# Optimization experiments

Hardware: AMD Instinct MI355X
Metric: run time of the kernel (lower is better)

## Reference

```python
import jax, jax.numpy as jnp
import numpy as np

EPS = 1e-6
BN_EPS = 1e-5
K = 20

def vn_linear(x, W):
    # x: (B, Cin, 3, ...), W: (Cout, Cin)
    return jnp.einsum('oc,bc...->bo...', W, x)

def vn_batchnorm(x, gamma, beta):
    # x: (B, C, 3, ...). BN (training-mode batch stats) over per-channel vector norms.
    n = jnp.linalg.norm(x, axis=2) + EPS               # (B, C, ...)
    red = (0,) + tuple(range(2, n.ndim))
    mu = n.mean(red, keepdims=True)
    var = ((n - mu) ** 2).mean(red, keepdims=True)     # biased var, as BatchNorm uses
    sh = (1, -1) + (1,) * (n.ndim - 2)
    nbn = (n - mu) / jnp.sqrt(var + BN_EPS) * gamma.reshape(sh) + beta.reshape(sh)
    return x / n[:, :, None] * nbn[:, :, None]

def vn_leaky(x, Wf, Wd, gamma, beta, ns):
    # VNLinearLeakyReLU: linear -> VN batchnorm -> direction-gated leaky relu
    p = vn_batchnorm(vn_linear(x, Wf), gamma, beta)
    d = vn_linear(x, Wd)
    dot = jnp.sum(p * d, axis=2, keepdims=True)
    dsq = jnp.sum(d * d, axis=2, keepdims=True) + EPS
    neg = p - (dot / dsq) * d
    return ns * p + (1.0 - ns) * jnp.where(dot >= 0, p, neg)

def graph_feature_cross(x, k):
    # x: (B, N, 3) -> edge features (B, 3, 3, N, k): [nbr - x, x, nbr x x]
    sq = jnp.sum(x * x, axis=-1)                        # (B, N)
    d2 = sq[:, :, None] + sq[:, None, :] - 2.0 * jnp.einsum('bnd,bmd->bnm', x, x)
    idx = jax.lax.top_k(-d2, k)[1]                      # (B, N, k) nearest incl. self
    nbr = jax.vmap(lambda pts, ind: pts[ind])(x, idx)   # (B, N, k, 3)
    c = jnp.broadcast_to(x[:, :, None, :], nbr.shape)
    cr = jnp.cross(nbr, c)
    feat = jnp.stack([nbr - c, c, cr], axis=3)          # (B, N, k, 3ch, 3)
    return jnp.transpose(feat, (0, 3, 4, 1, 2))         # (B, 3, 3, N, k)


def setup_inputs() -> dict:
    key = jax.random.key(0)
    ks = iter(jax.random.split(key, 40))
    def W(shape):
        return jax.random.normal(next(ks), shape, jnp.float32) * 0.05
    d = {'x': jax.random.normal(next(ks), (2, 2048, 3), jnp.float32)}
    d.update(
        Wf_pos=W((21, 3)), Wd_pos=W((21, 3)), g_pos=jnp.ones(21), be_pos=jnp.zeros(21),
        Wf1=W((21, 21)), Wd1=W((21, 21)), g1=jnp.ones(21), be1=jnp.zeros(21),
        Wf2=W((42, 21)), Wd2=W((42, 21)), g2=jnp.ones(42), be2=jnp.zeros(42),
        W3=W((170, 42)), g3=jnp.ones(170), be3=jnp.zeros(170),
        Ws1f=W((170, 340)), Ws1d=W((170, 340)), gs1=jnp.ones(170), bs1=jnp.zeros(170),
        Ws2f=W((85, 170)), Ws2d=W((85, 170)), gs2=jnp.ones(85), bs2=jnp.zeros(85),
        Wstd=W((3, 85)),
        Wt1=W((1020, 1020)), Wt2=W((1020, 1020)), Wt3=W((14450, 1020)), bt3=jnp.zeros(14450),
    )
    return d


def reference(x, Wf_pos, Wd_pos, g_pos, be_pos, Wf1, Wd1, g1, be1, Wf2, Wd2, g2, be2,
              W3, g3, be3, Ws1f, Ws1d, gs1, bs1, Ws2f, Ws2d, gs2, bs2, Wstd,
              Wt1, Wt2, Wt3, bt3):
    B, N, _ = x.shape
    feat = graph_feature_cross(x, K)                                   # (B,3,3,N,K)
    h = vn_leaky(feat, Wf_pos, Wd_pos, g_pos, be_pos, 0.0).mean(-1)    # (B,21,3,N) pool over k
    h = vn_leaky(h, Wf1, Wd1, g1, be1, 0.0)                            # (B,21,3,N)
    h = vn_leaky(h, Wf2, Wd2, g2, be2, 0.0)                            # (B,42,3,N)
    h = vn_batchnorm(vn_linear(h, W3), g3, be3)                        # (B,170,3,N)
    z = h.mean(-1)                                                     # (B,170,3)
    h = jnp.concatenate([h, jnp.broadcast_to(z[..., None], z.shape + (N,))], axis=1)  # (B,340,3,N)
    # VNStdFeature (normalize_frame=False, default negative_slope=0.2 inside)
    z0 = vn_leaky(h, Ws1f, Ws1d, gs1, bs1, 0.2)                        # (B,170,3,N)
    z0 = vn_leaky(z0, Ws2f, Ws2d, gs2, bs2, 0.2)                       # (B,85,3,N)
    z0 = vn_linear(z0, Wstd)                                           # (B,3,3,N)
    hs = jnp.einsum('bijn,bjkn->bikn', h, z0)                          # (B,340,3,N) invariant feats
    t = hs.reshape(B, 340 * 3, N)                                      # (B,1020,N)
    t = jax.nn.relu(jnp.einsum('oc,bcn->bon', Wt1, t))
    t = jax.nn.relu(jnp.einsum('oc,bcn->bon', Wt2, t))
    t = jnp.einsum('oc,bcn->bon', Wt3, t) + bt3[None, :, None]         # (B,14450,N)
    theta = t.reshape(B, 85, 170, N)
    return (z, theta)
```

## Files before the change

kernel.cpp:

```cpp
#include <hip/hip_runtime.h>
#include <cstdint>
#include <cstddef>

constexpr int   BB     = 2;
constexpr int   NN     = 2048;
constexpr int   KNB    = 20;
constexpr float EPS_   = 1e-6f;
constexpr float BNEPS_ = 1e-5f;
constexpr int   KPAD   = 1024;
constexpr int   NTK    = KPAD / 64;
constexpr int   MT3    = 57;
constexpr int   MPAD3  = MT3 * 256;

typedef __bf16 bf16x8 __attribute__((ext_vector_type(8)));
typedef float  f32x4  __attribute__((ext_vector_type(4)));

typedef const void t_gvoid __attribute__((address_space(1)));
typedef void       t_lvoid __attribute__((address_space(3)));

__device__ __forceinline__ unsigned short f2bf(float f) {
  unsigned int u = __builtin_bit_cast(unsigned int, f);
  u += 0x7FFFu + ((u >> 16) & 1u);
  return (unsigned short)(u >> 16);
}

__global__ __launch_bounds__(256) void knn_kernel(const float* __restrict__ x,
                                                  int* __restrict__ idx) {
  __shared__ float4 pts[NN];
  const int b = blockIdx.x >> 9;
  const int tid = threadIdx.x;
  const float* xb = x + (size_t)b * NN * 3;
  for (int i = tid; i < NN; i += 256) {
    float px = xb[i * 3], py = xb[i * 3 + 1], pz = xb[i * 3 + 2];
    pts[i] = make_float4(px, py, pz, px * px + py * py + pz * pz);
  }
  __syncthreads();
  const int wave = tid >> 6, lane = tid & 63;
  const int q = (blockIdx.x & 511) * 4 + wave;
  const float4 qp = pts[q];

  float d[32];
  #pragma unroll
  for (int i = 0; i < 32; ++i) {
    const float4 p = pts[lane + 64 * i];
    d[i] = qp.w + p.w - 2.0f * (qp.x * p.x + qp.y * p.y + qp.z * p.z);
  }

  float m; int mi;
  auto rescan = [&]() {
    m = 3.4e38f; mi = 0;
    #pragma unroll
    for (int i = 0; i < 32; ++i)
      if (d[i] < m) { m = d[i]; mi = i; }
  };
  rescan();

  int* op = idx + ((size_t)b * NN + q) * KNB;
  for (int r = 0; r < KNB; ++r) {
    float bm = m; int bj = lane + 64 * mi;
    #pragma unroll
    for (int s = 32; s > 0; s >>= 1) {
      const float om = __shfl_xor(bm, s, 64);
      const int   oj = __shfl_xor(bj, s, 64);
      if (om < bm || (om == bm && oj < bj)) { bm = om; bj = oj; }
    }
    if (lane == 0) op[r] = bj;
    if ((bj & 63) == lane) {
      const int ii = bj >> 6;
      #pragma unroll
      for (int i = 0; i < 32; ++i)
        if (i == ii) d[i] = 3.4e38f;
      rescan();
    }
  }
}

__global__ void feat_kernel(const float* __restrict__ x, const int* __restrict__ idx,
                            float* __restrict__ feat) {
  const int i = blockIdx.x * 256 + threadIdx.x;
  if (i >= BB * NN * KNB) return;
  const int n = (i / KNB) % NN, b = i / (KNB * NN);
  const float* xb = x + (size_t)b * NN * 3;
  const int j = idx[i];
  const float cx = xb[n * 3], cy = xb[n * 3 + 1], cz = xb[n * 3 + 2];
  const float nx = xb[j * 3], ny = xb[j * 3 + 1], nz = xb[j * 3 + 2];
  float* f = feat + (size_t)i * 9;
  f[0] = nx - cx; f[1] = ny - cy; f[2] = nz - cz;
  f[3] = cx;      f[4] = cy;      f[5] = cz;
  f[6] = ny * cz - nz * cy;
  f[7] = nz * cx - nx * cz;
  f[8] = nx * cy - ny * cx;
}

__global__ void l1_stats_part(const float* __restrict__ feat, const float* __restrict__ Wf,
                              float* __restrict__ part) {
  const int o = blockIdx.x, g = blockIdx.y, tid = threadIdx.x;
  const float w0 = Wf[o * 3], w1 = Wf[o * 3 + 1], w2 = Wf[o * 3 + 2];
  const int M = BB * NN * KNB;
  const int chunk = M / 8;
  float s1 = 0.f, s2 = 0.f;
  for (int i = g * chunk + tid; i < (g + 1) * chunk; i += 256) {
    const float* f = feat + (size_t)i * 9;
    float p0 = w0 * f[0] + w1 * f[3] + w2 * f[6];
    float p1 = w0 * f[1] + w1 * f[4] + w2 * f[7];
    float p2 = w0 * f[2] + w1 * f[5] + w2 * f[8];
    float nr = sqrtf(p0 * p0 + p1 * p1 + p2 * p2) + EPS_;
    s1 += nr; s2 += nr * nr;
  }
  __shared__ float rA[256], rB[256];
  rA[tid] = s1; rB[tid] = s2; __syncthreads();
  for (int off = 128; off > 0; off >>= 1) {
    if (tid < off) { rA[tid] += rA[tid + off]; rB[tid] += rB[tid + off]; }
    __syncthreads();
  }
  if (tid == 0) {
    part[(o * 8 + g) * 2]     = rA[0];
    part[(o * 8 + g) * 2 + 1] = rB[0];
  }
}

__global__ void l1_stats_fin(const float* __restrict__ part, const float* __restrict__ gamma,
                             float* __restrict__ stats) {
  const int o = threadIdx.x;
  if (o >= 21) return;
  const int M = BB * NN * KNB;
  float s1 = 0.f, s2 = 0.f;
  for (int g = 0; g < 8; ++g) { s1 += part[(o * 8 + g) * 2]; s2 += part[(o * 8 + g) * 2 + 1]; }
  float mu = s1 / M;
  float var = fmaxf(s2 / M - mu * mu, 0.f);
  stats[2 * o] = mu;
  stats[2 * o + 1] = gamma[o] / sqrtf(var + BNEPS_);
}

__global__ void l1_final_kernel(const float* __restrict__ feat, const float* __restrict__ Wf,
                                const float* __restrict__ Wd, const float* __restrict__ stats,
                                const float* __restrict__ beta, float* __restrict__ h1) {
  const int o = blockIdx.y, b = blockIdx.z;
  const int n = blockIdx.x * 256 + threadIdx.x;
  const float wf0 = Wf[o * 3], wf1 = Wf[o * 3 + 1], wf2 = Wf[o * 3 + 2];
  const float wd0 = Wd[o * 3], wd1 = Wd[o * 3 + 1], wd2 = Wd[o * 3 + 2];
  const float mu = stats[2 * o], sc = stats[2 * o + 1], be = beta[o];
  const float* fb = feat + ((size_t)(b * NN + n)) * KNB * 9;
  float a0 = 0.f, a1 = 0.f, a2 = 0.f;
  for (int k = 0; k < KNB; ++k) {
    const float* f = fb + k * 9;
    float p0 = wf0 * f[0] + wf1 * f[3] + wf2 * f[6];
    float p1 = wf0 * f[1] + wf1 * f[4] + wf2 * f[7];
    float p2 = wf0 * f[2] + wf1 * f[5] + wf2 * f[8];
    float d0 = wd0 * f[0] + wd1 * f[3] + wd2 * f[6];
    float d1 = wd0 * f[1] + wd1 * f[4] + wd2 * f[7];
    float d2 = wd0 * f[2] + wd1 * f[5] + wd2 * f[8];
    float nr = sqrtf(p0 * p0 + p1 * p1 + p2 * p2) + EPS_;
    float fac = ((nr - mu) * sc + be) / nr;
    p0 *= fac; p1 *= fac; p2 *= fac;
    float dot = p0 * d0 + p1 * d1 + p2 * d2;
    if (dot < 0.f) {
      float g = dot / (d0 * d0 + d1 * d1 + d2 * d2 + EPS_);
      p0 -= g * d0; p1 -= g * d1; p2 -= g * d2;
    }
    a0 += p0; a1 += p1; a2 += p2;
  }
  const size_t base = ((size_t)(b * 21 + o) * 3) * NN + n;
  h1[base]          = a0 * (1.f / KNB);
  h1[base + NN]     = a1 * (1.f / KNB);
  h1[base + 2 * NN] = a2 * (1.f / KNB);
}

__global__ void zbias_kernel(const float* __restrict__ zbuf, const float* __restrict__ Wf,
                             const float* __restrict__ Wd, float* __restrict__ zbf,
                             float* __restrict__ zbd, int Cout, int CinFull, int Cz) {
  const int bj = blockIdx.x;
  const int b = bj / 3, j = bj % 3;
  const int o = threadIdx.x;
  if (o >= Cout) return;
  const int off = CinFull - Cz;
  float sf = 0.f, sd = 0.f;
  for (int cz = 0; cz < Cz; ++cz) {
    const float zv = zbuf[((size_t)b * 170 + cz) * 3 + j];
    sf += Wf[(size_t)o * CinFull + off + cz] * zv;
    sd += Wd[(size_t)o * CinFull + off + cz] * zv;
  }
  zbf[(size_t)bj * Cout + o] = sf;
  zbd[(size_t)bj * Cout + o] = sd;
}

template <int HAS_D, int CONCAT_Z>
__global__ __launch_bounds__(256) void vn_lin_fast(
    const float* __restrict__ in, const float* __restrict__ Wf, const float* __restrict__ Wd,
    const float* __restrict__ zbf, const float* __restrict__ zbd,
    float* __restrict__ pout, float* __restrict__ dout,
    int Cin, int CinFull, int Cout) {
  __shared__ float wsh[(HAS_D ? 2 : 1) * 16 * 340];
  float* wfs = wsh;
  float* wds = HAS_D ? (wsh + 16 * 340) : wsh;
  const int tid = threadIdx.x;
  const int nt = blockIdx.x, ot = blockIdx.y;
  const int b = blockIdx.z / 3, j = blockIdx.z % 3;

  for (int i = tid; i < 16 * Cin; i += 256) {
    const int ol = i / Cin, c = i - ol * Cin;
    const int o = ot * 16 + ol;
    wfs[ol * Cin + c] = (o < Cout) ? Wf[(size_t)o * CinFull + c] : 0.f;
    if (HAS_D) wds[ol * Cin + c] = (o < Cout) ? Wd[(size_t)o * CinFull + c] : 0.f;
  }
  __syncthreads();

  const int lane = tid & 63, og = tid >> 6;
  const int n0 = nt * 256 + lane * 4;
  const float* ibase = in + ((size_t)b * Cin * 3 + j) * NN + n0;

  f32x4 accf[4], accd[4];
  #pragma unroll
  for (int oo = 0; oo < 4; ++oo) {
    float bf = 0.f, bd = 0.f;
    if (CONCAT_Z) {
      const int o = ot * 16 + og * 4 + oo;
      if (o < Cout) {
        bf = zbf[(size_t)blockIdx.z * Cout + o];
        bd = zbd[(size_t)blockIdx.z * Cout + o];
      }
    }
    accf[oo] = (f32x4){bf, bf, bf, bf};
    accd[oo] = (f32x4){bd, bd, bd, bd};
  }

  #pragma unroll 4
  for (int c = 0; c < Cin; ++c) {
    const f32x4 v = *reinterpret_cast<const f32x4*>(ibase + (size_t)c * 3 * NN);
    #pragma unroll
    for (int oo = 0; oo < 4; ++oo) {
      const float wf = wfs[(og * 4 + oo) * Cin + c];
      accf[oo] += wf * v;
      if (HAS_D) {
        const float wd = wds[(og * 4 + oo) * Cin + c];
        accd[oo] += wd * v;
      }
    }
  }

  #pragma unroll
  for (int oo = 0; oo < 4; ++oo) {
    const int o = ot * 16 + og * 4 + oo;
    if (o < Cout) {
      const size_t ob = ((size_t)(b * Cout + o) * 3 + j) * NN + n0;
      *reinterpret_cast<f32x4*>(pout + ob) = accf[oo];
      if (HAS_D) *reinterpret_cast<f32x4*>(dout + ob) = accd[oo];
    }
  }
}

__global__ void bn_stats_kernel(const float* __restrict__ p, const float* __restrict__ gamma,
                                float* __restrict__ stats, int Cout) {
  const int o = blockIdx.x, tid = threadIdx.x;
  const int M = BB * NN;
  float s1 = 0.f, s2 = 0.f;
  for (int i = tid; i < M; i += 256) {
    const int b = i >> 11, n = i & (NN - 1);
    const size_t base = (((size_t)(b * Cout + o)) * 3) * NN + n;
    float p0 = p[base], p1 = p[base + NN], p2 = p[base + 2 * NN];
    float nr = sqrtf(p0 * p0 + p1 * p1 + p2 * p2) + EPS_;
    s1 += nr; s2 += nr * nr;
  }
  __shared__ float rA[256], rB[256];
  rA[tid] = s1; rB[tid] = s2; __syncthreads();
  for (int off = 128; off > 0; off >>= 1) {
    if (tid < off) { rA[tid] += rA[tid + off]; rB[tid] += rB[tid + off]; }
    __syncthreads();
  }
  if (tid == 0) {
    float mu = rA[0] / M;
    float var = fmaxf(rB[0] / M - mu * mu, 0.f);
    stats[2 * o] = mu;
    stats[2 * o + 1] = gamma[o] / sqrtf(var + BNEPS_);
  }
}

template <int GATE>
__global__ void vn_gate_kernel(const float* __restrict__ p, const float* __restrict__ d,
                               const float* __restrict__ stats, const float* __restrict__ beta,
                               float* __restrict__ out, int Cout, float ns) {
  const int o = blockIdx.y, b = blockIdx.z;
  const int n = blockIdx.x * 256 + threadIdx.x;
  const size_t base = (((size_t)(b * Cout + o)) * 3) * NN + n;
  float p0 = p[base], p1 = p[base + NN], p2 = p[base + 2 * NN];
  const float nr = sqrtf(p0 * p0 + p1 * p1 + p2 * p2) + EPS_;
  const float fac = ((nr - stats[2 * o]) * stats[2 * o + 1] + beta[o]) / nr;
  p0 *= fac; p1 *= fac; p2 *= fac;
  float o0 = p0, o1 = p1, o2 = p2;
  if (GATE) {
    const float d0 = d[base], d1 = d[base + NN], d2 = d[base + 2 * NN];
    const float dot = p0 * d0 + p1 * d1 + p2 * d2;
    if (dot < 0.f) {
      const float g = dot / (d0 * d0 + d1 * d1 + d2 * d2 + EPS_);
      o0 = p0 - g * d0; o1 = p1 - g * d1; o2 = p2 - g * d2;
    }
    o0 = ns * p0 + (1.f - ns) * o0;
    o1 = ns * p1 + (1.f - ns) * o1;
    o2 = ns * p2 + (1.f - ns) * o2;
  }
  out[base] = o0; out[base + NN] = o1; out[base + 2 * NN] = o2;
}

__global__ void zmean_kernel(const float* __restrict__ h4, float* __restrict__ zbuf,
                             float* __restrict__ outz) {
  const int oj = blockIdx.x;
  const int b = blockIdx.y;
  const int tid = threadIdx.x;
  const float* src = h4 + ((size_t)b * 510 + oj) * NN;
  float s = 0.f;
  for (int n = tid; n < NN; n += 256) s += src[n];
  __shared__ float r[256];
  r[tid] = s; __syncthreads();
  for (int off = 128; off > 0; off >>= 1) {
    if (tid < off) r[tid] += r[tid + off];
    __syncthreads();
  }
  if (tid == 0) {
    float m = r[0] / NN;
    zbuf[(size_t)b * 510 + oj] = m;
    outz[(size_t)b * 510 + oj] = m;
  }
}

__global__ void hs_kernel(const float* __restrict__ h4, const float* __restrict__ zbuf,
                          const float* __restrict__ z0f, unsigned short* __restrict__ t0) {
  const int n = blockIdx.x;
  const int b = blockIdx.z;
  const int tid = threadIdx.x;
  __shared__ float zf[9];
  if (tid < 9) zf[tid] = z0f[(((size_t)(b * 3 + tid / 3)) * 3 + (tid % 3)) * NN + n];
  __syncthreads();
  unsigned short* trow = t0 + ((size_t)b * NN + n) * KPAD;
  for (int c = tid; c < KPAD; c += 256) {
    if (c >= 1020) { trow[c] = 0; continue; }
    const int i = c / 3, kv = c % 3;
    float acc = 0.f;
    #pragma unroll
    for (int j = 0; j < 3; ++j) {
      float hv = (i < 170) ? h4[(((size_t)(b * 170 + i)) * 3 + j) * NN + n]
                           : zbuf[(size_t)b * 510 + (i - 170) * 3 + j];
      acc += hv * zf[j * 3 + kv];
    }
    trow[c] = f2bf(acc);
  }
}

__global__ void wconv_kernel(const float* __restrict__ W, unsigned short* __restrict__ out,
                             int M, int Kv, size_t total) {
  size_t i = (size_t)blockIdx.x * 256 + threadIdx.x;
  const size_t stride = (size_t)gridDim.x * 256;
  for (; i < total; i += stride) {
    const int k = (int)(i & (KPAD - 1));
    const int o = (int)(i >> 10);
    out[i] = (o < M && k < Kv) ? f2bf(W[(size_t)o * Kv + k]) : (unsigned short)0;
  }
}

template <int RELU>
__global__ __launch_bounds__(256) void gemm_kernel(
    const unsigned short* __restrict__ A, const unsigned short* __restrict__ Bmat,
    unsigned short* __restrict__ outB, int M) {
  __shared__ __align__(16) unsigned short lA[2][128 * 64];
  __shared__ __align__(16) unsigned short lB[2][128 * 64];
  const int tid = threadIdx.x;
  const int nwg = gridDim.x, q = nwg >> 3;
  const int orig = blockIdx.x;
  const int swz = (orig & 7) * q + (orig >> 3);
  const int ntile = swz & 15;
  const int mtile = (swz >> 4) & 7;
  const int b = swz >> 7;
  const int lane = tid & 63, w = tid >> 6;
  const int wm = w >> 1, wn = w & 1;
  const int lrow = lane & 15, lgrp = lane >> 4;

  const unsigned short* Abase = A + (size_t)mtile * 128 * KPAD;
  const unsigned short* Bbase = Bmat + ((size_t)b * NN + (size_t)ntile * 128) * KPAD;

  const int rowS = tid >> 3;
  const int scol = ((tid & 7) * 8) ^ ((rowS & 7) * 8);
  const int wb8  = __builtin_amdgcn_readfirstlane(tid & 192) * 8;

  f32x4 acc[4][4];
  #pragma unroll
  for (int mi = 0; mi < 4; ++mi)
    #pragma unroll
    for (int ni = 0; ni < 4; ++ni) acc[mi][ni] = (f32x4){0.f, 0.f, 0.f, 0.f};

  auto stage = [&](int bufi, int kt) {
    const int kof = kt * 64;
    #pragma unroll
    for (int r = 0; r < 4; ++r) {
      __builtin_amdgcn_global_load_lds(
          (t_gvoid*)(Abase + (size_t)(r * 32 + rowS) * KPAD + kof + scol),
          (t_lvoid*)&lA[bufi][r * 2048 + wb8], 16, 0, 0);
      __builtin_amdgcn_global_load_lds(
          (t_gvoid*)(Bbase + (size_t)(r * 32 + rowS) * KPAD + kof + scol),
          (t_lvoid*)&lB[bufi][r * 2048 + wb8], 16, 0, 0);
    }
  };

  stage(0, 0);
  for (int kt = 0; kt < NTK; ++kt) {
    const int cur = kt & 1;
    if (kt + 1 < NTK) {
      stage(cur ^ 1, kt + 1);
      asm volatile("s_waitcnt vmcnt(8)" ::: "memory");
    } else {
      asm volatile("s_waitcnt vmcnt(0)" ::: "memory");
    }
    asm volatile("s_barrier" ::: "memory");

    bf16x8 af[4][2], bfr[4][2];
    #pragma unroll
    for (int mi = 0; mi < 4; ++mi) {
      const int ra = wm * 64 + mi * 16 + lrow;
      const int rb = wn * 64 + mi * 16 + lrow;
      #pragma unroll
      for (int kk = 0; kk < 2; ++kk) {
        af[mi][kk]  = *reinterpret_cast<const bf16x8*>(
            &lA[cur][ra * 64 + ((kk * 32 + lgrp * 8) ^ ((ra & 7) * 8))]);
        bfr[mi][kk] = *reinterpret_cast<const bf16x8*>(
            &lB[cur][rb * 64 + ((kk * 32 + lgrp * 8) ^ ((rb & 7) * 8))]);
      }
    }
    #pragma unroll
    for (int kk = 0; kk < 2; ++kk)
      #pragma unroll
      for (int mi = 0; mi < 4; ++mi)
        #pragma unroll
        for (int ni = 0; ni < 4; ++ni)
          acc[mi][ni] = __builtin_amdgcn_mfma_f32_16x16x32_bf16(af[mi][kk], bfr[ni][kk],
                                                                acc[mi][ni], 0, 0, 0);
    asm volatile("s_barrier" ::: "memory");
  }

  const int fr_col = lane & 15;
  const int fr_rowb = (lane >> 4) * 4;
  #pragma unroll
  for (int mi = 0; mi < 4; ++mi) {
    const int rowb = mtile * 128 + wm * 64 + mi * 16 + fr_rowb;
    #pragma unroll
    for (int ni = 0; ni < 4; ++ni) {
      const int col = ntile * 128 + wn * 64 + ni * 16 + fr_col;
      ushort4 v;
      if (rowb < M) {
        float u0 = acc[mi][ni][0], u1 = acc[mi][ni][1], u2 = acc[mi][ni][2], u3 = acc[mi][ni][3];
        if (RELU) { u0 = fmaxf(u0, 0.f); u1 = fmaxf(u1, 0.f); u2 = fmaxf(u2, 0.f); u3 = fmaxf(u3, 0.f); }
        v.x = f2bf(u0); v.y = f2bf(u1); v.z = f2bf(u2); v.w = f2bf(u3);
      } else {
        v.x = v.y = v.z = v.w = 0;
      }
      *reinterpret_cast<ushort4*>(outB + ((size_t)b * NN + col) * KPAD + rowb) = v;
    }
  }
}

__global__ __launch_bounds__(512, 2) void gemm256_kernel(
    const unsigned short* __restrict__ A, const unsigned short* __restrict__ Bmat,
    float* __restrict__ outF, const float* __restrict__ bias, int M, int MT) {
  __shared__ __align__(16) unsigned short lA[2][256 * 64];
  __shared__ __align__(16) unsigned short lB[2][256 * 64];
  const int tid = threadIdx.x;
  const int nwg = gridDim.x, q = nwg >> 3;
  const int orig = blockIdx.x;
  const int swz = (orig & 7) * q + (orig >> 3);
  const int ntile = swz & 7;
  const int rem = swz >> 3;
  const int mtile = rem % MT;
  const int b = rem / MT;
  const int lane = tid & 63, w = tid >> 6;
  const int wm = w >> 2, wn = w & 3;
  const int lrow = lane & 15, lgrp = lane >> 4;

  const unsigned short* Abase = A + (size_t)mtile * 256 * KPAD;
  const unsigned short* Bbase = Bmat + ((size_t)b * NN + (size_t)ntile * 256) * KPAD;

  const int rowS = tid >> 3;
  const int scol = ((tid & 7) * 8) ^ ((rowS & 7) * 8);
  const int wb8  = __builtin_amdgcn_readfirstlane((tid & 448) >> 6) * 512;

  f32x4 acc[8][4];
  #pragma unroll
  for (int mi = 0; mi < 8; ++mi)
    #pragma unroll
    for (int ni = 0; ni < 4; ++ni) acc[mi][ni] = (f32x4){0.f, 0.f, 0.f, 0.f};

  auto stage = [&](int bufi, int kt) {
    const int kof = kt * 64;
    #pragma unroll
    for (int r = 0; r < 4; ++r) {
      __builtin_amdgcn_global_load_lds(
          (t_gvoid*)(Abase + (size_t)(r * 64 + rowS) * KPAD + kof + scol),
          (t_lvoid*)&lA[bufi][r * 4096 + wb8], 16, 0, 0);
      __builtin_amdgcn_global_load_lds(
          (t_gvoid*)(Bbase + (size_t)(r * 64 + rowS) * KPAD + kof + scol),
          (t_lvoid*)&lB[bufi][r * 4096 + wb8], 16, 0, 0);
    }
  };

  stage(0, 0);
  for (int kt = 0; kt < NTK; ++kt) {
    const int cur = kt & 1;
    if (kt + 1 < NTK) {
      stage(cur ^ 1, kt + 1);
      asm volatile("s_waitcnt vmcnt(8)" ::: "memory");
    } else {
      asm volatile("s_waitcnt vmcnt(0)" ::: "memory");
    }
    asm volatile("s_barrier" ::: "memory");

    #pragma unroll
    for (int kk = 0; kk < 2; ++kk) {
      bf16x8 af[8], bfr[4];
      #pragma unroll
      for (int mi = 0; mi < 8; ++mi) {
        const int ra = wm * 128 + mi * 16 + lrow;
        af[mi] = *reinterpret_cast<const bf16x8*>(
            &lA[cur][ra * 64 + ((kk * 32 + lgrp * 8) ^ ((ra & 7) * 8))]);
      }
      #pragma unroll
      for (int ni = 0; ni < 4; ++ni) {
        const int rb = wn * 64 + ni * 16 + lrow;
        bfr[ni] = *reinterpret_cast<const bf16x8*>(
            &lB[cur][rb * 64 + ((kk * 32 + lgrp * 8) ^ ((rb & 7) * 8))]);
      }
      #pragma unroll
      for (int mi = 0; mi < 8; ++mi)
        #pragma unroll
        for (int ni = 0; ni < 4; ++ni)
          acc[mi][ni] = __builtin_amdgcn_mfma_f32_16x16x32_bf16(af[mi], bfr[ni],
                                                                acc[mi][ni], 0, 0, 0);
    }
    asm volatile("s_barrier" ::: "memory");
  }

  const int fr_col = lane & 15;
  const int fr_rowb = (lane >> 4) * 4;
  #pragma unroll
  for (int mi = 0; mi < 8; ++mi) {
    const int rowb = mtile * 256 + wm * 128 + mi * 16 + fr_rowb;
    #pragma unroll
    for (int ni = 0; ni < 4; ++ni) {
      const int col = ntile * 256 + wn * 64 + ni * 16 + fr_col;
      #pragma unroll
      for (int r = 0; r < 4; ++r) {
        const int rr = rowb + r;
        if (rr < M) outF[((size_t)b * M + rr) * NN + col] = acc[mi][ni][r] + bias[rr];
      }
    }
  }
}

extern "C" void kernel_launch(void* const* d_in, const int* in_sizes, int n_in,
                              void* d_out, int out_size, void* d_ws, size_t ws_size,
                              hipStream_t stream) {
  const float* x      = (const float*)d_in[0];
  const float* Wf_pos = (const float*)d_in[1];
  const float* Wd_pos = (const float*)d_in[2];
  const float* g_pos  = (const float*)d_in[3];
  const float* be_pos = (const float*)d_in[4];
  const float* Wf1    = (const float*)d_in[5];
  const float* Wd1    = (const float*)d_in[6];
  const float* g1     = (const float*)d_in[7];
  const float* be1    = (const float*)d_in[8];
  const float* Wf2    = (const float*)d_in[9];
  const float* Wd2    = (const float*)d_in[10];
  const float* g2     = (const float*)d_in[11];
  const float* be2    = (const float*)d_in[12];
  const float* W3     = (const float*)d_in[13];
  const float* g3     = (const float*)d_in[14];
  const float* be3    = (const float*)d_in[15];
  const float* Ws1f   = (const float*)d_in[16];
  const float* Ws1d   = (const float*)d_in[17];
  const float* gs1    = (const float*)d_in[18];
  const float* bs1    = (const float*)d_in[19];
  const float* Ws2f   = (const float*)d_in[20];
  const float* Ws2d   = (const float*)d_in[21];
  const float* gs2    = (const float*)d_in[22];
  const float* bs2    = (const float*)d_in[23];
  const float* Wstd   = (const float*)d_in[24];
  const float* Wt1    = (const float*)d_in[25];
  const float* Wt2    = (const float*)d_in[26];
  const float* Wt3    = (const float*)d_in[27];
  const float* bt3    = (const float*)d_in[28];
  (void)in_sizes; (void)n_in; (void)out_size; (void)ws_size;

  float* out = (float*)d_out;
  float* out_theta = out + 1020;

  char* ws = (char*)d_ws;
  size_t off = 0;
  auto alloc = [&](size_t bytes) -> void* {
    void* p = (void*)(ws + off);
    off += (bytes + 255) & ~(size_t)255;
    return p;
  };
  int*            idx  = (int*)           alloc((size_t)BB * NN * KNB * 4);
  float*          feat = (float*)         alloc((size_t)BB * NN * KNB * 9 * 4);
  float*          stats= (float*)         alloc(1024 * 4);
  float*          part = (float*)         alloc(2048 * 4);
  float*          h1   = (float*)         alloc((size_t)BB * 21 * 3 * NN * 4);
  float*          h2   = (float*)         alloc((size_t)BB * 21 * 3 * NN * 4);
  float*          h3   = (float*)         alloc((size_t)BB * 42 * 3 * NN * 4);
  float*          h4   = (float*)         alloc((size_t)BB * 170 * 3 * NN * 4);
  float*          zbuf = (float*)         alloc((size_t)BB * 170 * 3 * 4);
  float*          pbuf = (float*)         alloc((size_t)BB * 170 * 3 * NN * 4);
  float*          dbuf = (float*)         alloc((size_t)BB * 170 * 3 * NN * 4);
  float*          z0a  = (float*)         alloc((size_t)BB * 170 * 3 * NN * 4);
  float*          z0b  = (float*)         alloc((size_t)BB * 85 * 3 * NN * 4);
  float*          z0f  = (float*)         alloc((size_t)BB * 3 * 3 * NN * 4);
  float*          zbf  = (float*)         alloc((size_t)6 * 170 * 4);
  float*          zbd  = (float*)         alloc((size_t)6 * 170 * 4);
  unsigned short* W1b  = (unsigned short*)alloc((size_t)1024 * KPAD * 2);
  unsigned short* W2b  = (unsigned short*)alloc((size_t)1024 * KPAD * 2);
  unsigned short* W3b  = (unsigned short*)alloc((size_t)MPAD3 * KPAD * 2);
  unsigned short* t0   = (unsigned short*)alloc((size_t)BB * NN * KPAD * 2);
  unsigned short* t1   = (unsigned short*)alloc((size_t)BB * NN * KPAD * 2);
  unsigned short* t2   = t0;

  knn_kernel<<<BB * 512, 256, 0, stream>>>(x, idx);
  feat_kernel<<<(BB * NN * KNB + 255) / 256, 256, 0, stream>>>(x, idx, feat);
  l1_stats_part<<<dim3(21, 8), 256, 0, stream>>>(feat, Wf_pos, part);
  l1_stats_fin<<<1, 64, 0, stream>>>(part, g_pos, stats);
  l1_final_kernel<<<dim3(8, 21, BB), 256, 0, stream>>>(feat, Wf_pos, Wd_pos, stats, be_pos, h1);

  vn_lin_fast<1, 0><<<dim3(8, 2, BB * 3), 256, 0, stream>>>(h1, Wf1, Wd1, nullptr, nullptr, pbuf, dbuf, 21, 21, 21);
  bn_stats_kernel<<<21, 256, 0, stream>>>(pbuf, g1, stats, 21);
  vn_gate_kernel<1><<<dim3(8, 21, BB), 256, 0, stream>>>(pbuf, dbuf, stats, be1, h2, 21, 0.0f);

  vn_lin_fast<1, 0><<<dim3(8, 3, BB * 3), 256, 0, stream>>>(h2, Wf2, Wd2, nullptr, nullptr, pbuf, dbuf, 21, 21, 42);
  bn_stats_kernel<<<42, 256, 0, stream>>>(pbuf, g2, stats, 42);
  vn_gate_kernel<1><<<dim3(8, 42, BB), 256, 0, stream>>>(pbuf, dbuf, stats, be2, h3, 42, 0.0f);

  vn_lin_fast<0, 0><<<dim3(8, 11, BB * 3), 256, 0, stream>>>(h3, W3, nullptr, nullptr, nullptr, pbuf, nullptr, 42, 42, 170);
  bn_stats_kernel<<<170, 256, 0, stream>>>(pbuf, g3, stats, 170);
  vn_gate_kernel<0><<<dim3(8, 170, BB), 256, 0, stream>>>(pbuf, nullptr, stats, be3, h4, 170, 0.0f);

  zmean_kernel<<<dim3(510, BB), 256, 0, stream>>>(h4, zbuf, out);

  zbias_kernel<<<6, 256, 0, stream>>>(zbuf, Ws1f, Ws1d, zbf, zbd, 170, 340, 170);
  vn_lin_fast<1, 1><<<dim3(8, 11, BB * 3), 256, 0, stream>>>(h4, Ws1f, Ws1d, zbf, zbd, pbuf, dbuf, 170, 340, 170);
  bn_stats_kernel<<<170, 256, 0, stream>>>(pbuf, gs1, stats, 170);
  vn_gate_kernel<1><<<dim3(8, 170, BB), 256, 0, stream>>>(pbuf, dbuf, stats, bs1, z0a, 170, 0.2f);

  vn_lin_fast<1, 0><<<dim3(8, 6, BB * 3), 256, 0, stream>>>(z0a, Ws2f, Ws2d, nullptr, nullptr, pbuf, dbuf, 170, 170, 85);
  bn_stats_kernel<<<85, 256, 0, stream>>>(pbuf, gs2, stats, 85);
  vn_gate_kernel<1><<<dim3(8, 85, BB), 256, 0, stream>>>(pbuf, dbuf, stats, bs2, z0b, 85, 0.2f);

  vn_lin_fast<0, 0><<<dim3(8, 1, BB * 3), 256, 0, stream>>>(z0b, Wstd, nullptr, nullptr, nullptr, z0f, nullptr, 85, 85, 3);

  hs_kernel<<<dim3(NN, 1, BB), 256, 0, stream>>>(h4, zbuf, z0f, t0);

  wconv_kernel<<<1024, 256, 0, stream>>>(Wt1, W1b, 1020, 1020, (size_t)1024 * KPAD);
  wconv_kernel<<<1024, 256, 0, stream>>>(Wt2, W2b, 1020, 1020, (size_t)1024 * KPAD);
  wconv_kernel<<<2048, 256, 0, stream>>>(Wt3, W3b, 14450, 1020, (size_t)MPAD3 * KPAD);

  gemm_kernel<1><<<256, 256, 0, stream>>>(W1b, t0, t1, 1020);
  gemm_kernel<1><<<256, 256, 0, stream>>>(W2b, t1, t2, 1020);
  gemm256_kernel<<<8 * MT3 * BB, 512, 0, stream>>>(W3b, t2, out_theta, bt3, 14450, MT3);
}
```

Baseline: 568.1 us.

## Interleave staged global-to-LDS loads with MFMA phases in big GEMM

Restructures the 256x256 GEMM main loop into four sub-phases per K tile. Each phase reads A/B fragments from LDS, issues a quarter of the next tile's global-to-LDS loads, and runs half the MFMAs under raised wave priority. The aim is to spread memory traffic across the compute and keep the matrix cores busy. In exchange there are more barriers per K tile and a full vmcnt(0) wait at the end of each tile.

```diff
diff --git a/kernel.cpp b/kernel.cpp
--- a/kernel.cpp
+++ b/kernel.cpp
@@ -461,9 +461,9 @@
   __shared__ __align__(16) unsigned short lA[2][256 * 64];
   __shared__ __align__(16) unsigned short lB[2][256 * 64];
   const int tid = threadIdx.x;
-  const int nwg = gridDim.x, q = nwg >> 3;
+  const int nwg = gridDim.x, q0 = nwg >> 3;
   const int orig = blockIdx.x;
-  const int swz = (orig & 7) * q + (orig >> 3);
+  const int swz = (orig & 7) * q0 + (orig >> 3);
   const int ntile = swz & 7;
   const int rem = swz >> 3;
   const int mtile = rem % MT;
@@ -475,8 +475,8 @@
   const unsigned short* Abase = A + (size_t)mtile * 256 * KPAD;
   const unsigned short* Bbase = Bmat + ((size_t)b * NN + (size_t)ntile * 256) * KPAD;
 
-  const int rowS = tid >> 3;
-  const int scol = ((tid & 7) * 8) ^ ((rowS & 7) * 8);
+  const int rowH = tid >> 3;
+  const int scol = ((tid & 7) * 8) ^ ((rowH & 7) * 8);
   const int wb8  = __builtin_amdgcn_readfirstlane((tid & 448) >> 6) * 512;
 
   f32x4 acc[8][4];
@@ -485,53 +485,58 @@
     #pragma unroll
     for (int ni = 0; ni < 4; ++ni) acc[mi][ni] = (f32x4){0.f, 0.f, 0.f, 0.f};
 
-  auto stage = [&](int bufi, int kt) {
+  auto stage_half = [&](int bufi, int kt, int h) {
     const int kof = kt * 64;
-    #pragma unroll
-    for (int r = 0; r < 4; ++r) {
+    const unsigned short* base = (h < 2) ? Abase : Bbase;
+    const int hr = (h & 1) * 128;
+    unsigned short* ldsb = ((h < 2) ? &lA[bufi][0] : &lB[bufi][0]) + hr * 64;
+    #pragma unroll
+    for (int r = 0; r < 2; ++r) {
       __builtin_amdgcn_global_load_lds(
-          (t_gvoid*)(Abase + (size_t)(r * 64 + rowS) * KPAD + kof + scol),
-          (t_lvoid*)&lA[bufi][r * 4096 + wb8], 16, 0, 0);
-      __builtin_amdgcn_global_load_lds(
-          (t_gvoid*)(Bbase + (size_t)(r * 64 + rowS) * KPAD + kof + scol),
-          (t_lvoid*)&lB[bufi][r * 4096 + wb8], 16, 0, 0);
+          (t_gvoid*)(base + (size_t)(hr + r * 64 + rowH) * KPAD + kof + scol),
+          (t_lvoid*)(ldsb + r * 4096 + wb8), 16, 0, 0);
     }
   };
 
-  stage(0, 0);
+  #pragma unroll
+  for (int h = 0; h < 4; ++h) stage_half(0, 0, h);
+  asm volatile("s_waitcnt vmcnt(0)" ::: "memory");
+  asm volatile("s_barrier" ::: "memory");
+
   for (int kt = 0; kt < NTK; ++kt) {
     const int cur = kt & 1;
-    if (kt + 1 < NTK) {
-      stage(cur ^ 1, kt + 1);
-      asm volatile("s_waitcnt vmcnt(8)" ::: "memory");
-    } else {
-      asm volatile("s_waitcnt vmcnt(0)" ::: "memory");
-    }
-    asm volatile("s_barrier" ::: "memory");
-
-    #pragma unroll
-    for (int kk = 0; kk < 2; ++kk) {
-      bf16x8 af[8], bfr[4];
+    bf16x8 bfr[4];
+    #pragma unroll
+    for (int qq = 0; qq < 4; ++qq) {
+      const int kk = qq >> 1, mh = qq & 1;
+      bf16x8 af[4];
+      if (mh == 0) {
+        #pragma unroll
+        for (int ni = 0; ni < 4; ++ni) {
+          const int rb = wn * 64 + ni * 16 + lrow;
+          bfr[ni] = *reinterpret_cast<const bf16x8*>(
+              &lB[cur][rb * 64 + ((kk * 32 + lgrp * 8) ^ ((rb & 7) * 8))]);
+        }
+      }
       #pragma unroll
-      for (int mi = 0; mi < 8; ++mi) {
-        const int ra = wm * 128 + mi * 16 + lrow;
+      for (int mi = 0; mi < 4; ++mi) {
+        const int ra = wm * 128 + mh * 64 + mi * 16 + lrow;
         af[mi] = *reinterpret_cast<const bf16x8*>(
             &lA[cur][ra * 64 + ((kk * 32 + lgrp * 8) ^ ((ra & 7) * 8))]);
       }
+      if (kt + 1 < NTK) stage_half(cur ^ 1, kt + 1, qq);
+      asm volatile("s_barrier" ::: "memory");
+      __builtin_amdgcn_s_setprio(1);
       #pragma unroll
-      for (int ni = 0; ni < 4; ++ni) {
-        const int rb = wn * 64 + ni * 16 + lrow;
-        bfr[ni] = *reinterpret_cast<const bf16x8*>(
-            &lB[cur][rb * 64 + ((kk * 32 + lgrp * 8) ^ ((rb & 7) * 8))]);
-      }
-      #pragma unroll
-      for (int mi = 0; mi < 8; ++mi)
+      for (int mi = 0; mi < 4; ++mi)
         #pragma unroll
         for (int ni = 0; ni < 4; ++ni)
-          acc[mi][ni] = __builtin_amdgcn_mfma_f32_16x16x32_bf16(af[mi], bfr[ni],
-                                                                acc[mi][ni], 0, 0, 0);
-    }
-    asm volatile("s_barrier" ::: "memory");
+          acc[mh * 4 + mi][ni] = __builtin_amdgcn_mfma_f32_16x16x32_bf16(
+              af[mi], bfr[ni], acc[mh * 4 + mi][ni], 0, 0, 0);
+      __builtin_amdgcn_s_setprio(0);
+      if (qq == 3) asm volatile("s_waitcnt vmcnt(0)" ::: "memory");
+      asm volatile("s_barrier" ::: "memory");
+    }
   }
 
   const int fr_col = lane & 15;
```

Measured after the change: 575.4 us. No clear change (+1.3%).

## Halve gemm256 K-tile to 32 for higher occupancy; stage hs inputs in LDS

Applied to the files above, without the earlier changes.

The big 256x256 GEMM now stages K-tiles of 32 instead of 64, halving LDS per block, and reworks the swizzle and fragment loads to match. Launch bounds are raised to 4 waves-per-SIMD hint and fragment loads are interleaved with MFMAs to cut register pressure, aiming for more resident blocks and better latency hiding. The cost is twice as many barriers and pipeline stages per K loop. The hs kernel also caches each column of h4 and zbuf in shared memory to avoid repeated strided global loads.

```diff
diff --git a/kernel.cpp b/kernel.cpp
--- a/kernel.cpp
+++ b/kernel.cpp
@@ -9,6 +9,7 @@
 constexpr float BNEPS_ = 1e-5f;
 constexpr int   KPAD   = 1024;
 constexpr int   NTK    = KPAD / 64;
+constexpr int   NTK32  = KPAD / 32;
 constexpr int   MT3    = 57;
 constexpr int   MPAD3  = MT3 * 256;
 
@@ -328,7 +329,13 @@
   const int b = blockIdx.z;
   const int tid = threadIdx.x;
   __shared__ float zf[9];
+  __shared__ float hcol[512];
+  __shared__ float zcol[512];
   if (tid < 9) zf[tid] = z0f[(((size_t)(b * 3 + tid / 3)) * 3 + (tid % 3)) * NN + n];
+  for (int i = tid; i < 510; i += 256) {
+    hcol[i] = h4[((size_t)b * 510 + i) * NN + n];
+    zcol[i] = zbuf[(size_t)b * 510 + i];
+  }
   __syncthreads();
   unsigned short* trow = t0 + ((size_t)b * NN + n) * KPAD;
   for (int c = tid; c < KPAD; c += 256) {
@@ -337,8 +344,7 @@
     float acc = 0.f;
     #pragma unroll
     for (int j = 0; j < 3; ++j) {
-      float hv = (i < 170) ? h4[(((size_t)(b * 170 + i)) * 3 + j) * NN + n]
-                           : zbuf[(size_t)b * 510 + (i - 170) * 3 + j];
+      const float hv = (i < 170) ? hcol[i * 3 + j] : zcol[(i - 170) * 3 + j];
       acc += hv * zf[j * 3 + kv];
     }
     trow[c] = f2bf(acc);
@@ -455,15 +461,15 @@
   }
 }
 
-__global__ __launch_bounds__(512, 2) void gemm256_kernel(
+__global__ __launch_bounds__(512, 4) void gemm256_kernel(
     const unsigned short* __restrict__ A, const unsigned short* __restrict__ Bmat,
     float* __restrict__ outF, const float* __restrict__ bias, int M, int MT) {
-  __shared__ __align__(16) unsigned short lA[2][256 * 64];
-  __shared__ __align__(16) unsigned short lB[2][256 * 64];
+  __shared__ __align__(16) unsigned short lA[2][256 * 32];
+  __shared__ __align__(16) unsigned short lB[2][256 * 32];
   const int tid = threadIdx.x;
-  const int nwg = gridDim.x, q = nwg >> 3;
+  const int nwg = gridDim.x, q0 = nwg >> 3;
   const int orig = blockIdx.x;
-  const int swz = (orig & 7) * q + (orig >> 3);
+  const int swz = (orig & 7) * q0 + (orig >> 3);
   const int ntile = swz & 7;
   const int rem = swz >> 3;
   const int mtile = rem % MT;
@@ -475,9 +481,9 @@
   const unsigned short* Abase = A + (size_t)mtile * 256 * KPAD;
   const unsigned short* Bbase = Bmat + ((size_t)b * NN + (size_t)ntile * 256) * KPAD;
 
-  const int rowS = tid >> 3;
-  const int scol = ((tid & 7) * 8) ^ ((rowS & 7) * 8);
-  const int wb8  = __builtin_amdgcn_readfirstlane((tid & 448) >> 6) * 512;
+  const int rowT = tid >> 2;
+  const int scol = (((tid & 3) ^ (rowT & 3)) * 8);
+  const int wbase = __builtin_amdgcn_readfirstlane((tid & 448) >> 6) * 512;
 
   f32x4 acc[8][4];
   #pragma unroll
@@ -486,50 +492,44 @@
     for (int ni = 0; ni < 4; ++ni) acc[mi][ni] = (f32x4){0.f, 0.f, 0.f, 0.f};
 
   auto stage = [&](int bufi, int kt) {
-    const int kof = kt * 64;
-    #pragma unroll
-    for (int r = 0; r < 4; ++r) {
+    const int kof = kt * 32;
+    #pragma unroll
+    for (int r = 0; r < 2; ++r) {
       __builtin_amdgcn_global_load_lds(
-          (t_gvoid*)(Abase + (size_t)(r * 64 + rowS) * KPAD + kof + scol),
-          (t_lvoid*)&lA[bufi][r * 4096 + wb8], 16, 0, 0);
+          (t_gvoid*)(Abase + (size_t)(r * 128 + rowT) * KPAD + kof + scol),
+          (t_lvoid*)&lA[bufi][r * 4096 + wbase], 16, 0, 0);
       __builtin_amdgcn_global_load_lds(
-          (t_gvoid*)(Bbase + (size_t)(r * 64 + rowS) * KPAD + kof + scol),
-          (t_lvoid*)&lB[bufi][r * 4096 + wb8], 16, 0, 0);
+          (t_gvoid*)(Bbase + (size_t)(r * 128 + rowT) * KPAD + kof + scol),
+          (t_lvoid*)&lB[bufi][r * 4096 + wbase], 16, 0, 0);
     }
   };
 
   stage(0, 0);
-  for (int kt = 0; kt < NTK; ++kt) {
+  for (int kt = 0; kt < NTK32; ++kt) {
     const int cur = kt & 1;
-    if (kt + 1 < NTK) {
+    if (kt + 1 < NTK32) {
       stage(cur ^ 1, kt + 1);
-      asm volatile("s_waitcnt vmcnt(8)" ::: "memory");
+      asm volatile("s_waitcnt vmcnt(4)" ::: "memory");
     } else {
       asm volatile("s_waitcnt vmcnt(0)" ::: "memory");
     }
     asm volatile("s_barrier" ::: "memory");
 
-    #pragma unroll
-    for (int kk = 0; kk < 2; ++kk) {
-      bf16x8 af[8], bfr[4];
+    bf16x8 bfr[4];
+    #pragma unroll
+    for (int ni = 0; ni < 4; ++ni) {
+      const int rb = wn * 64 + ni * 16 + lrow;
+      bfr[ni] = *reinterpret_cast<const bf16x8*>(
+          &lB[cur][rb * 32 + ((lgrp ^ (rb & 3)) * 8)]);
+    }
+    #pragma unroll
+    for (int mi = 0; mi < 8; ++mi) {
+      const int ra = wm * 128 + mi * 16 + lrow;
+      const bf16x8 a = *reinterpret_cast<const bf16x8*>(
+          &lA[cur][ra * 32 + ((lgrp ^ (ra & 3)) * 8)]);
       #pragma unroll
-      for (int mi = 0; mi < 8; ++mi) {
-        const int ra = wm * 128 + mi * 16 + lrow;
-        af[mi] = *reinterpret_cast<const bf16x8*>(
-            &lA[cur][ra * 64 + ((kk * 32 + lgrp * 8) ^ ((ra & 7) * 8))]);
-      }
-      #pragma unroll
-      for (int ni = 0; ni < 4; ++ni) {
-        const int rb = wn * 64 + ni * 16 + lrow;
-        bfr[ni] = *reinterpret_cast<const bf16x8*>(
-            &lB[cur][rb * 64 + ((kk * 32 + lgrp * 8) ^ ((rb & 7) * 8))]);
-      }
-      #pragma unroll
-      for (int mi = 0; mi < 8; ++mi)
-        #pragma unroll
-        for (int ni = 0; ni < 4; ++ni)
-          acc[mi][ni] = __builtin_amdgcn_mfma_f32_16x16x32_bf16(af[mi], bfr[ni],
-                                                                acc[mi][ni], 0, 0, 0);
+      for (int ni = 0; ni < 4; ++ni)
+        acc[mi][ni] = __builtin_amdgcn_mfma_f32_16x16x32_bf16(a, bfr[ni], acc[mi][ni], 0, 0, 0);
     }
     asm volatile("s_barrier" ::: "memory");
   }
```

Measured after the change: 1.021 ms. +79.8%, slower.
